# Performance work log

Measured on AMD Instinct MI355X. Metric: run time of the kernel, lower is better.

The kernel has to match this reference:

```python
import jax, jax.numpy as jnp
import numpy as np

ITEM_NUM = 100000
H = 128          # hidden_size
L_PROTO = 500    # number of prototypes
K = 4            # top-k prototypes
SEQ = 50         # max_seq_length
B = 1024
TAO = 0.1
LAMBDA = 0.1
EPS = 1e-5


def layer_norm(x, g, b):
    mu = jnp.mean(x, axis=-1, keepdims=True)
    var = jnp.mean((x - mu) ** 2, axis=-1, keepdims=True)
    return (x - mu) * jax.lax.rsqrt(var + EPS) * g + b


def setup_inputs() -> dict:
    key = jax.random.key(0)
    ks = jax.random.split(key, 12)
    std = 0.02
    item_emb = jax.random.normal(ks[0], (ITEM_NUM, H), jnp.float32) * std
    item_emb = item_emb.at[0].set(0.0)  # padding_idx=0
    pos_emb = jax.random.normal(ks[1], (SEQ + 1, H), jnp.float32) * std
    pos_emb = pos_emb.at[0].set(0.0)    # padding_idx=0 (never hit when len==SEQ)
    proto = jax.random.normal(ks[2], (L_PROTO, H), jnp.float32) * std
    w1 = jax.random.normal(ks[3], (H, H), jnp.float32) * std
    w2 = jax.random.normal(ks[4], (H, 1), jnp.float32) * std
    w3 = jax.random.normal(ks[5], (H, H), jnp.float32) * std
    w4 = jax.random.normal(ks[6], (H, H), jnp.float32) * std
    w5 = jax.random.normal(ks[7], (H, K), jnp.float32) * std
    w6 = jax.random.normal(ks[8], (H, H), jnp.float32) * std
    w7 = jax.random.normal(ks[9], (H, 1), jnp.float32) * std
    seq = jax.random.randint(ks[10], (B, SEQ), 0, ITEM_NUM, dtype=jnp.int64)
    g = jnp.ones((H,), jnp.float32)
    b = jnp.zeros((H,), jnp.float32)
    return {
        'item_emb': item_emb, 'pos_emb': pos_emb, 'proto': proto,
        'w1': w1, 'w2': w2, 'w3': w3, 'w4': w4, 'w5': w5, 'w6': w6, 'w7': w7,
        'ln1_g': g, 'ln1_b': b, 'ln2_g': g, 'ln2_b': b,
        'ln3_g': g, 'ln3_b': b, 'ln4_g': g, 'ln4_b': b,
        'seq': seq,
    }


def reference(item_emb, pos_emb, proto, w1, w2, w3, w4, w5, w6, w7,
              ln1_g, ln1_b, ln2_g, ln2_b, ln3_g, ln3_b, ln4_g, ln4_b, seq):
    mask = (seq != 0).astype(jnp.float32)            # [B,S]
    ie = item_emb[seq]                               # [B,S,H]

    # self-attentive virtual concept vector
    sa_score = jnp.squeeze(jnp.tanh(ie @ w1) @ w2, -1)   # [B,S]
    sa_score = sa_score - (1.0 - mask) * 10000.0
    alpha = jax.nn.softmax(sa_score, axis=-1)
    vcv = jnp.einsum('bs,bsh->bh', alpha, ie)            # [B,H]

    # prototype routing: top-k by score
    s = vcv @ proto.T                                    # [B,L]
    chosen_s, rank = jax.lax.top_k(s, K)                 # [B,K]
    chosen_proto = proto[rank]                           # [B,K,H]
    chosen_proto = jax.nn.sigmoid(chosen_s)[..., None] * chosen_proto

    # item->prototype assignment
    p_kt_score = jnp.einsum('bsh,bkh->bsk',
                            layer_norm(ie @ w3, ln1_g, ln1_b),
                            layer_norm(chosen_proto, ln2_g, ln2_b))
    p_kt = jax.nn.softmax(p_kt_score, axis=-1) * mask[:, :, None]  # [B,S,K]

    # positional embedding (positions SEQ..1)
    position = SEQ - jnp.arange(SEQ)                     # [S]
    emb = pos_emb[position][None, :, :] + ie             # [B,S,H]

    a_k_score = jnp.swapaxes(jnp.tanh(emb @ w4) @ w5, 1, 2)   # [B,K,S]
    a_k = jax.nn.softmax(a_k_score, axis=-1) * mask[:, None, :]
    a_k = jnp.swapaxes(a_k, 1, 2)                        # [B,S,K]

    p = p_kt * a_k
    interesting = layer_norm(jnp.einsum('bsk,bsh->bkh', p, emb), ln3_g, ln3_b)  # [B,K,H]

    xu = jnp.einsum('bsk,bkh->bsh', p_kt, chosen_proto)  # [B,S,H]
    c_score = jnp.squeeze(jnp.tanh(xu @ w6) @ w7, -1) - (1.0 - mask) * 10000.0
    c_w = jax.nn.softmax(c_score, axis=-1)               # [B,S]
    c_apt = layer_norm(jnp.einsum('bs,bsh->bh', c_w, xu), ln4_g, ln4_b)  # [B,H]

    e_score = jnp.einsum('bh,bkh->bk', c_apt, interesting)
    e = jax.nn.softmax(e_score / TAO, axis=-1)
    final = jnp.einsum('bk,bkh->bh', e, interesting)     # [B,H]
    scores = final @ item_emb.T                          # [B,ITEM_NUM]

    # prototype covariance regularizer
    centered = proto - jnp.mean(proto, axis=0, keepdims=True)
    M = (centered @ centered.T) / H
    Lc = (jnp.linalg.norm(M) - jnp.linalg.norm(jnp.diag(M))) * 0.5
    return scores, LAMBDA * Lc
```

## Files before the change

kernel.cpp:

```cpp
#include <hip/hip_runtime.h>
#include <hip/hip_bf16.h>

#define H 128
#define H2 132
#define SQL 50
#define LPROTO 500
#define KTOP 4
#define BQ 1024
#define ITEMS 100000

typedef __attribute__((ext_vector_type(8))) short bf16x8;
typedef __attribute__((ext_vector_type(4))) float f32x4;

__device__ __forceinline__ float wsum(float v){
#pragma unroll
  for (int o = 32; o; o >>= 1) v += __shfl_xor(v, o, 64);
  return v;
}
__device__ __forceinline__ float wmax(float v){
#pragma unroll
  for (int o = 32; o; o >>= 1) v = fmaxf(v, __shfl_xor(v, o, 64));
  return v;
}
__device__ __forceinline__ float gr16(float v){
  v += __shfl_xor(v, 1, 64);
  v += __shfl_xor(v, 2, 64);
  v += __shfl_xor(v, 4, 64);
  v += __shfl_xor(v, 8, 64);
  return v;
}
__device__ __forceinline__ unsigned short f2bf(float x){
  unsigned int u = __builtin_bit_cast(unsigned int, x);
  unsigned int r = u + 0x7fffu + ((u >> 16) & 1u);
  return (unsigned short)(r >> 16);
}
__device__ __forceinline__ float bf2f(unsigned short h){
  unsigned int u = ((unsigned int)h) << 16;
  return __builtin_bit_cast(float, u);
}
__device__ __forceinline__ float ftanh(float x){
  float e = __expf(-2.0f * fabsf(x));
  float t = (1.0f - e) / (1.0f + e);
  return copysignf(t, x);
}

__device__ __forceinline__ void mm_core(const float xs[4][8],
                                        const unsigned short* __restrict__ wt_hi,
                                        const unsigned short* __restrict__ wt_lo,
                                        int r15, int kof, f32x4* acc)
{
  bf16x8 ah[4], al[4];
#pragma unroll
  for (int ks = 0; ks < 4; ks++){
    bf16x8 h, l;
#pragma unroll
    for (int e = 0; e < 8; e++){
      unsigned short hb = f2bf(xs[ks][e]);
      float rem = xs[ks][e] - bf2f(hb);
      h[e] = (short)hb;
      l[e] = (short)f2bf(rem);
    }
    ah[ks] = h; al[ks] = l;
  }
#pragma unroll
  for (int j = 0; j < 8; j++){
    const unsigned short* bp = wt_hi + (j * 16 + r15) * H + kof;
    const unsigned short* lp = wt_lo + (j * 16 + r15) * H + kof;
    f32x4 a = (f32x4){0.f, 0.f, 0.f, 0.f};
#pragma unroll
    for (int ks = 0; ks < 4; ks++){
      bf16x8 bh = *reinterpret_cast<const bf16x8*>(bp + ks * 32);
      bf16x8 bl = *reinterpret_cast<const bf16x8*>(lp + ks * 32);
      a = __builtin_amdgcn_mfma_f32_16x16x32_bf16(ah[ks], bh, a, 0, 0, 0);
      a = __builtin_amdgcn_mfma_f32_16x16x32_bf16(al[ks], bh, a, 0, 0, 0);
      a = __builtin_amdgcn_mfma_f32_16x16x32_bf16(ah[ks], bl, a, 0, 0, 0);
    }
    acc[j] = a;
  }
}

__device__ __forceinline__ void mm_acc(const float (*src)[H2],
                                       const unsigned short* __restrict__ wt_hi,
                                       const unsigned short* __restrict__ wt_lo,
                                       int lane, int wave, f32x4* acc)
{
  const int r15 = lane & 15, g = lane >> 4, kof = g * 8;
  const int row = wave * 16 + r15;
  const int srw = (row < SQL) ? row : 0;
  float xs[4][8];
#pragma unroll
  for (int ks = 0; ks < 4; ks++){
    const float* p = &src[srw][ks * 32 + kof];
    float4 x0 = *reinterpret_cast<const float4*>(p);
    float4 x1 = *reinterpret_cast<const float4*>(p + 4);
    xs[ks][0]=x0.x; xs[ks][1]=x0.y; xs[ks][2]=x0.z; xs[ks][3]=x0.w;
    xs[ks][4]=x1.x; xs[ks][5]=x1.y; xs[ks][6]=x1.z; xs[ks][7]=x1.w;
  }
  mm_core(xs, wt_hi, wt_lo, r15, kof, acc);
}

__device__ __forceinline__ void mm_acc_pos(const float (*src)[H2],
                                           const float* __restrict__ pos_emb,
                                           const unsigned short* __restrict__ wt_hi,
                                           const unsigned short* __restrict__ wt_lo,
                                           int lane, int wave, f32x4* acc)
{
  const int r15 = lane & 15, g = lane >> 4, kof = g * 8;
  const int row = wave * 16 + r15;
  const int srw = (row < SQL) ? row : 0;
  const float* pp = pos_emb + (SQL - srw) * H;
  float xs[4][8];
#pragma unroll
  for (int ks = 0; ks < 4; ks++){
    const float* p = &src[srw][ks * 32 + kof];
    float4 x0 = *reinterpret_cast<const float4*>(p);
    float4 x1 = *reinterpret_cast<const float4*>(p + 4);
    float4 p0 = *reinterpret_cast<const float4*>(pp + ks * 32 + kof);
    float4 p1 = *reinterpret_cast<const float4*>(pp + ks * 32 + kof + 4);
    xs[ks][0]=x0.x+p0.x; xs[ks][1]=x0.y+p0.y; xs[ks][2]=x0.z+p0.z; xs[ks][3]=x0.w+p0.w;
    xs[ks][4]=x1.x+p1.x; xs[ks][5]=x1.y+p1.y; xs[ks][6]=x1.z+p1.z; xs[ks][7]=x1.w+p1.w;
  }
  mm_core(xs, wt_hi, wt_lo, r15, kof, acc);
}

extern "C" __global__ __launch_bounds__(256, 4)
void sine_row(const float* __restrict__ item_emb, const float* __restrict__ pos_emb,
              const float* __restrict__ proto,
              const float* __restrict__ w2, const float* __restrict__ w5,
              const float* __restrict__ w7,
              const unsigned short* __restrict__ wt,
              const float* __restrict__ ln1g, const float* __restrict__ ln1b,
              const float* __restrict__ ln2g, const float* __restrict__ ln2b,
              const float* __restrict__ ln3g, const float* __restrict__ ln3b,
              const float* __restrict__ ln4g, const float* __restrict__ ln4b,
              const int* __restrict__ seq,
              unsigned short* __restrict__ finalbf)
{
  __shared__ __align__(16) float sA[SQL][H2];
  __shared__ __align__(16) float scp[KTOP][H];
  __shared__ __align__(16) float slncp[KTOP][H];
  __shared__ __align__(16) float sintr[KTOP][H];
  __shared__ __align__(16) float svcv[H];
  __shared__ __align__(16) float scapt[H];
  __shared__ float srow[SQL];
  __shared__ float smask[SQL];
  __shared__ float spkt[SQL][KTOP];
  __shared__ float sak[SQL][KTOP];
  __shared__ float ssc[LPROTO];
  __shared__ float schs[KTOP];
  __shared__ int   srank[KTOP];
  __shared__ float sesc[KTOP];

  const int b = blockIdx.x;
  const int t = threadIdx.x;
  const int lane = t & 63;
  const int wave = t >> 6;
  const int r15 = lane & 15;
  const int g   = lane >> 4;
  const int* sq = seq + b * SQL;

  const unsigned short* w1t_hi = wt;
  const unsigned short* w1t_lo = wt + 16384;
  const unsigned short* w3t_hi = wt + 32768;
  const unsigned short* w3t_lo = wt + 49152;
  const unsigned short* w4t_hi = wt + 65536;
  const unsigned short* w4t_lo = wt + 81920;
  const unsigned short* w6t_hi = wt + 98304;
  const unsigned short* w6t_lo = wt + 114688;

  if (t < SQL) smask[t] = (sq[t] != 0) ? 1.0f : 0.0f;
  for (int c = t; c < SQL * (H / 4); c += 256){
    int s = c >> 5, q = c & 31;
    int idx = sq[s];
    float4 v = reinterpret_cast<const float4*>(item_emb)[idx * (H / 4) + q];
    reinterpret_cast<float4*>(&sA[s][0])[q] = v;
  }
  __syncthreads();

  {
    f32x4 acc[8];
    mm_acc(sA, w1t_hi, w1t_lo, lane, wave, acc);
    float p0 = 0.f, p1 = 0.f, p2 = 0.f, p3 = 0.f;
#pragma unroll
    for (int j = 0; j < 8; j++){
      float w2c = w2[j * 16 + r15];
      p0 = fmaf(ftanh(acc[j][0]), w2c, p0);
      p1 = fmaf(ftanh(acc[j][1]), w2c, p1);
      p2 = fmaf(ftanh(acc[j][2]), w2c, p2);
      p3 = fmaf(ftanh(acc[j][3]), w2c, p3);
    }
    p0 = gr16(p0); p1 = gr16(p1); p2 = gr16(p2); p3 = gr16(p3);
    if (r15 == 0){
      float pv[4] = {p0, p1, p2, p3};
#pragma unroll
      for (int r = 0; r < 4; r++){
        int orow = wave * 16 + g * 4 + r;
        if (orow < SQL) srow[orow] = pv[r] - (1.0f - smask[orow]) * 10000.0f;
      }
    }
  }
  __syncthreads();

  if (wave == 0){
    float v = (lane < SQL) ? srow[lane] : -1e30f;
    float m = wmax(v);
    float e = (lane < SQL) ? __expf(v - m) : 0.0f;
    float sum = wsum(e);
    if (lane < SQL) srow[lane] = e / sum;
  }
  __syncthreads();
  if (t < H){
    float acc = 0.f;
    for (int s = 0; s < SQL; s++) acc = fmaf(srow[s], sA[s][t], acc);
    svcv[t] = acc;
  }
  __syncthreads();

  for (int l = t; l < LPROTO; l += 256){
    const float4* pr = reinterpret_cast<const float4*>(proto + l * H);
    const float4* vc = reinterpret_cast<const float4*>(svcv);
    float acc = 0.f;
    for (int q = 0; q < H / 4; q++){
      float4 p = pr[q], v = vc[q];
      acc += p.x * v.x + p.y * v.y + p.z * v.z + p.w * v.w;
    }
    ssc[l] = acc;
  }
  __syncthreads();
  if (wave == 0){
    float cand[8];
#pragma unroll
    for (int i = 0; i < 8; i++){
      int l = lane + 64 * i;
      cand[i] = (l < LPROTO) ? ssc[l] : -1e30f;
    }
    for (int k = 0; k < KTOP; k++){
      float bv = -1e30f; int bi = 0x7fffffff;
#pragma unroll
      for (int i = 0; i < 8; i++){
        int l = lane + 64 * i;
        if (cand[i] > bv || (cand[i] == bv && l < bi)){ bv = cand[i]; bi = l; }
      }
#pragma unroll
      for (int o = 32; o; o >>= 1){
        float ov = __shfl_xor(bv, o, 64);
        int   oi = __shfl_xor(bi, o, 64);
        if (ov > bv || (ov == bv && oi < bi)){ bv = ov; bi = oi; }
      }
      if (lane == 0){ schs[k] = bv; srank[k] = bi; }
      int li = bi - lane;
#pragma unroll
      for (int i = 0; i < 8; i++) if (64 * i == li) cand[i] = -1e30f;
    }
  }
  __syncthreads();
  {
    int k = wave;
    int r = srank[k];
    float sg = 1.0f / (1.0f + __expf(-schs[k]));
    float v0 = sg * proto[r * H + lane];
    float v1 = sg * proto[r * H + 64 + lane];
    float mu = wsum(v0 + v1) * (1.0f / H);
    float d0 = v0 - mu, d1 = v1 - mu;
    float var = wsum(d0 * d0 + d1 * d1) * (1.0f / H);
    float rs = rsqrtf(var + 1e-5f);
    scp[k][lane] = v0; scp[k][64 + lane] = v1;
    slncp[k][lane]      = d0 * rs * ln2g[lane]      + ln2b[lane];
    slncp[k][64 + lane] = d1 * rs * ln2g[64 + lane] + ln2b[64 + lane];
  }
  __syncthreads();

  {
    f32x4 acc[8];
    mm_acc(sA, w3t_hi, w3t_lo, lane, wave, acc);
    float s0 = 0.f, s1 = 0.f, s2 = 0.f, s3 = 0.f;
#pragma unroll
    for (int j = 0; j < 8; j++){ s0 += acc[j][0]; s1 += acc[j][1]; s2 += acc[j][2]; s3 += acc[j][3]; }
    float mu0 = gr16(s0) * (1.0f / H), mu1 = gr16(s1) * (1.0f / H);
    float mu2 = gr16(s2) * (1.0f / H), mu3 = gr16(s3) * (1.0f / H);
    float q0 = 0.f, q1 = 0.f, q2 = 0.f, q3 = 0.f;
#pragma unroll
    for (int j = 0; j < 8; j++){
      float d0 = acc[j][0] - mu0, d1 = acc[j][1] - mu1;
      float d2 = acc[j][2] - mu2, d3 = acc[j][3] - mu3;
      q0 = fmaf(d0, d0, q0); q1 = fmaf(d1, d1, q1);
      q2 = fmaf(d2, d2, q2); q3 = fmaf(d3, d3, q3);
    }
    float rs0 = rsqrtf(gr16(q0) * (1.0f / H) + 1e-5f);
    float rs1 = rsqrtf(gr16(q1) * (1.0f / H) + 1e-5f);
    float rs2 = rsqrtf(gr16(q2) * (1.0f / H) + 1e-5f);
    float rs3 = rsqrtf(gr16(q3) * (1.0f / H) + 1e-5f);
    float pk[4][4];
#pragma unroll
    for (int k = 0; k < 4; k++)
#pragma unroll
      for (int r = 0; r < 4; r++) pk[k][r] = 0.f;
#pragma unroll
    for (int j = 0; j < 8; j++){
      int c = j * 16 + r15;
      float gg = ln1g[c], bb = ln1b[c];
      float l0 = fmaf((acc[j][0] - mu0) * rs0, gg, bb);
      float l1 = fmaf((acc[j][1] - mu1) * rs1, gg, bb);
      float l2 = fmaf((acc[j][2] - mu2) * rs2, gg, bb);
      float l3 = fmaf((acc[j][3] - mu3) * rs3, gg, bb);
#pragma unroll
      for (int k = 0; k < 4; k++){
        float w = slncp[k][c];
        pk[k][0] = fmaf(l0, w, pk[k][0]);
        pk[k][1] = fmaf(l1, w, pk[k][1]);
        pk[k][2] = fmaf(l2, w, pk[k][2]);
        pk[k][3] = fmaf(l3, w, pk[k][3]);
      }
    }
#pragma unroll
    for (int k = 0; k < 4; k++)
#pragma unroll
      for (int r = 0; r < 4; r++) pk[k][r] = gr16(pk[k][r]);
    if (r15 == 0){
#pragma unroll
      for (int r = 0; r < 4; r++){
        int orow = wave * 16 + g * 4 + r;
        if (orow < SQL){
          float m = fmaxf(fmaxf(pk[0][r], pk[1][r]), fmaxf(pk[2][r], pk[3][r]));
          float e0 = __expf(pk[0][r] - m), e1 = __expf(pk[1][r] - m);
          float e2 = __expf(pk[2][r] - m), e3 = __expf(pk[3][r] - m);
          float inv = 1.0f / (e0 + e1 + e2 + e3);
          float msk = smask[orow];
          spkt[orow][0] = e0 * inv * msk; spkt[orow][1] = e1 * inv * msk;
          spkt[orow][2] = e2 * inv * msk; spkt[orow][3] = e3 * inv * msk;
        }
      }
    }
  }
  __syncthreads();

  {
    f32x4 acc[8];
    mm_acc_pos(sA, pos_emb, w4t_hi, w4t_lo, lane, wave, acc);
    float pk[4][4];
#pragma unroll
    for (int k = 0; k < 4; k++)
#pragma unroll
      for (int r = 0; r < 4; r++) pk[k][r] = 0.f;
#pragma unroll
    for (int j = 0; j < 8; j++){
      int c = j * 16 + r15;
      float4 w5c = *reinterpret_cast<const float4*>(w5 + c * 4);
      float t0 = ftanh(acc[j][0]), t1 = ftanh(acc[j][1]);
      float t2 = ftanh(acc[j][2]), t3 = ftanh(acc[j][3]);
      pk[0][0] = fmaf(t0, w5c.x, pk[0][0]); pk[0][1] = fmaf(t1, w5c.x, pk[0][1]);
      pk[0][2] = fmaf(t2, w5c.x, pk[0][2]); pk[0][3] = fmaf(t3, w5c.x, pk[0][3]);
      pk[1][0] = fmaf(t0, w5c.y, pk[1][0]); pk[1][1] = fmaf(t1, w5c.y, pk[1][1]);
      pk[1][2] = fmaf(t2, w5c.y, pk[1][2]); pk[1][3] = fmaf(t3, w5c.y, pk[1][3]);
      pk[2][0] = fmaf(t0, w5c.z, pk[2][0]); pk[2][1] = fmaf(t1, w5c.z, pk[2][1]);
      pk[2][2] = fmaf(t2, w5c.z, pk[2][2]); pk[2][3] = fmaf(t3, w5c.z, pk[2][3]);
      pk[3][0] = fmaf(t0, w5c.w, pk[3][0]); pk[3][1] = fmaf(t1, w5c.w, pk[3][1]);
      pk[3][2] = fmaf(t2, w5c.w, pk[3][2]); pk[3][3] = fmaf(t3, w5c.w, pk[3][3]);
    }
#pragma unroll
    for (int k = 0; k < 4; k++)
#pragma unroll
      for (int r = 0; r < 4; r++) pk[k][r] = gr16(pk[k][r]);
    if (r15 == 0){
#pragma unroll
      for (int r = 0; r < 4; r++){
        int orow = wave * 16 + g * 4 + r;
        if (orow < SQL){
          sak[orow][0] = pk[0][r]; sak[orow][1] = pk[1][r];
          sak[orow][2] = pk[2][r]; sak[orow][3] = pk[3][r];
        }
      }
    }
  }
  __syncthreads();

  {
    int k = wave;
    float v = (lane < SQL) ? sak[lane][k] : -1e30f;
    float m = wmax(v);
    float e = (lane < SQL) ? __expf(v - m) : 0.0f;
    float sum = wsum(e);
    if (lane < SQL) sak[lane][k] = (e / sum) * smask[lane] * spkt[lane][k];
  }
  __syncthreads();

  for (int c = t; c < KTOP * H; c += 256){
    int k = c >> 7, h = c & 127;
    float acc = 0.f;
    for (int s = 0; s < SQL; s++)
      acc = fmaf(sak[s][k], sA[s][h] + pos_emb[(SQL - s) * H + h], acc);
    sintr[k][h] = acc;
  }
  __syncthreads();
  {
    int k = wave;
    float v0 = sintr[k][lane], v1 = sintr[k][64 + lane];
    float mu = wsum(v0 + v1) * (1.0f / H);
    float d0 = v0 - mu, d1 = v1 - mu;
    float var = wsum(d0 * d0 + d1 * d1) * (1.0f / H);
    float rs = rsqrtf(var + 1e-5f);
    sintr[k][lane]      = d0 * rs * ln3g[lane]      + ln3b[lane];
    sintr[k][64 + lane] = d1 * rs * ln3g[64 + lane] + ln3b[64 + lane];
  }
  __syncthreads();

  for (int c = t; c < SQL * H; c += 256){
    int s = c >> 7, h = c & 127;
    float acc = spkt[s][0] * scp[0][h] + spkt[s][1] * scp[1][h]
              + spkt[s][2] * scp[2][h] + spkt[s][3] * scp[3][h];
    sA[s][h] = acc;
  }
  __syncthreads();
  {
    f32x4 acc[8];
    mm_acc(sA, w6t_hi, w6t_lo, lane, wave, acc);
    float p0 = 0.f, p1 = 0.f, p2 = 0.f, p3 = 0.f;
#pragma unroll
    for (int j = 0; j < 8; j++){
      float w7c = w7[j * 16 + r15];
      p0 = fmaf(ftanh(acc[j][0]), w7c, p0);
      p1 = fmaf(ftanh(acc[j][1]), w7c, p1);
      p2 = fmaf(ftanh(acc[j][2]), w7c, p2);
      p3 = fmaf(ftanh(acc[j][3]), w7c, p3);
    }
    p0 = gr16(p0); p1 = gr16(p1); p2 = gr16(p2); p3 = gr16(p3);
    if (r15 == 0){
      float pv[4] = {p0, p1, p2, p3};
#pragma unroll
      for (int r = 0; r < 4; r++){
        int orow = wave * 16 + g * 4 + r;
        if (orow < SQL) srow[orow] = pv[r] - (1.0f - smask[orow]) * 10000.0f;
      }
    }
  }
  __syncthreads();

  if (wave == 0){
    float v = (lane < SQL) ? srow[lane] : -1e30f;
    float m = wmax(v);
    float e = (lane < SQL) ? __expf(v - m) : 0.0f;
    float sum = wsum(e);
    if (lane < SQL) srow[lane] = e / sum;
  }
  __syncthreads();
  if (t < H){
    float acc = 0.f;
    for (int s = 0; s < SQL; s++) acc = fmaf(srow[s], sA[s][t], acc);
    scapt[t] = acc;
  }
  __syncthreads();
  if (wave == 0){
    float v0 = scapt[lane], v1 = scapt[64 + lane];
    float mu = wsum(v0 + v1) * (1.0f / H);
    float d0 = v0 - mu, d1 = v1 - mu;
    float var = wsum(d0 * d0 + d1 * d1) * (1.0f / H);
    float rs = rsqrtf(var + 1e-5f);
    scapt[lane]      = d0 * rs * ln4g[lane]      + ln4b[lane];
    scapt[64 + lane] = d1 * rs * ln4g[64 + lane] + ln4b[64 + lane];
  }
  __syncthreads();

  {
    int k = wave;
    float part = scapt[lane] * sintr[k][lane] + scapt[64 + lane] * sintr[k][64 + lane];
    float sc = wsum(part);
    if (lane == 0) sesc[k] = sc;
  }
  __syncthreads();
  if (t < H){
    float e0 = sesc[0] * 10.0f, e1 = sesc[1] * 10.0f, e2 = sesc[2] * 10.0f, e3 = sesc[3] * 10.0f;
    float m = fmaxf(fmaxf(e0, e1), fmaxf(e2, e3));
    float x0 = __expf(e0 - m), x1 = __expf(e1 - m), x2 = __expf(e2 - m), x3 = __expf(e3 - m);
    float inv = 1.0f / (x0 + x1 + x2 + x3);
    float f = (x0 * sintr[0][t] + x1 * sintr[1][t] + x2 * sintr[2][t] + x3 * sintr[3][t]) * inv;
    finalbf[b * H + t] = f2bf(f);
  }
}

extern "C" __global__ void wprep(const float* __restrict__ w1, const float* __restrict__ w3,
                                 const float* __restrict__ w4, const float* __restrict__ w6,
                                 unsigned short* __restrict__ out){
  const float* srcs[4] = {w1, w3, w4, w6};
  const float* src = srcs[blockIdx.x];
  unsigned short* hi = out + blockIdx.x * 32768;
  unsigned short* lo = hi + 16384;
  for (int i = threadIdx.x; i < 16384; i += 256){
    int c = i >> 7, k = i & 127;
    float f = src[k * H + c];
    unsigned short h = f2bf(f);
    hi[i] = h;
    lo[i] = f2bf(f - bf2f(h));
  }
}

extern "C" __global__ void conv_bf16(const float* __restrict__ in,
                                     unsigned short* __restrict__ out, int n4){
  int i = blockIdx.x * blockDim.x + threadIdx.x;
  int stride = gridDim.x * blockDim.x;
  for (; i < n4; i += stride){
    float4 v = reinterpret_cast<const float4*>(in)[i];
    union { unsigned short u[4]; uint2 v2; } o;
    o.u[0] = f2bf(v.x); o.u[1] = f2bf(v.y); o.u[2] = f2bf(v.z); o.u[3] = f2bf(v.w);
    reinterpret_cast<uint2*>(out)[i] = o.v2;
  }
}

#define GBN 128
#define LDT 136

extern "C" __global__ __launch_bounds__(256)
void gemm_scores(const unsigned short* __restrict__ A,
                 const unsigned short* __restrict__ Bm,
                 float* __restrict__ C)
{
  __shared__ __align__(16) unsigned short sB[GBN][LDT];
  const int t = threadIdx.x, lane = t & 63, wave = t >> 6;
  const int r15 = lane & 15, g = lane >> 4;
  const int n0 = blockIdx.x * GBN;

  for (int c = t; c < GBN * 16; c += 256){
    int r = c >> 4, q = c & 15;
    int n = n0 + r;
    uint4 v = make_uint4(0u, 0u, 0u, 0u);
    if (n < ITEMS) v = reinterpret_cast<const uint4*>(Bm + (size_t)n * H)[q];
    *reinterpret_cast<uint4*>(&sB[r][q * 8]) = v;
  }
  __syncthreads();

  for (int mt = 0; mt < BQ / 128; mt++){
    const int m0 = mt * 128 + wave * 32;
    f32x4 acc[2][8];
#pragma unroll
    for (int i = 0; i < 2; i++)
#pragma unroll
      for (int j = 0; j < 8; j++) acc[i][j] = (f32x4){0.f, 0.f, 0.f, 0.f};

#pragma unroll
    for (int ks = 0; ks < 4; ks++){
      bf16x8 af[2];
#pragma unroll
      for (int i = 0; i < 2; i++)
        af[i] = *reinterpret_cast<const bf16x8*>(A + (m0 + i * 16 + r15) * H + ks * 32 + g * 8);
#pragma unroll
      for (int j = 0; j < 8; j++){
        bf16x8 bfr = *reinterpret_cast<const bf16x8*>(&sB[j * 16 + r15][ks * 32 + g * 8]);
        acc[0][j] = __builtin_amdgcn_mfma_f32_16x16x32_bf16(af[0], bfr, acc[0][j], 0, 0, 0);
        acc[1][j] = __builtin_amdgcn_mfma_f32_16x16x32_bf16(af[1], bfr, acc[1][j], 0, 0, 0);
      }
    }

#pragma unroll
    for (int i = 0; i < 2; i++){
      int mrow = m0 + i * 16 + g * 4;
#pragma unroll
      for (int j = 0; j < 8; j++){
        int nc = n0 + j * 16 + r15;
        if (nc < ITEMS){
#pragma unroll
          for (int r = 0; r < 4; r++)
            C[(size_t)(mrow + r) * ITEMS + nc] = acc[i][j][r];
        }
      }
    }
  }
}

extern "C" __global__ void proto_mean(const float* __restrict__ proto,
                                      float* __restrict__ mean, float* __restrict__ accum){
  __shared__ float part[4][H];
  int t = threadIdx.x;
  int h = t & 127, p = t >> 7;
  if (t < 2) accum[t] = 0.0f;
  float acc = 0.f;
  for (int l = p; l < LPROTO; l += 4) acc += proto[l * H + h];
  part[p][h] = acc;
  __syncthreads();
  if (t < H) mean[t] = (part[0][t] + part[1][t] + part[2][t] + part[3][t]) * (1.0f / LPROTO);
}

extern "C" __global__ __launch_bounds__(256)
void proto_cov(const float* __restrict__ proto, const float* __restrict__ mean,
               float* __restrict__ accum){
  __shared__ float ci[H];
  __shared__ float cm[H];
  __shared__ float red[256];
  int i = blockIdx.x, t = threadIdx.x;
  if (t < H){ cm[t] = mean[t]; ci[t] = proto[i * H + t] - mean[t]; }
  __syncthreads();
  float total = 0.f;
  for (int j = t; j < LPROTO; j += 256){
    float acc = 0.f;
    for (int h = 0; h < H; h++) acc = fmaf(ci[h], proto[j * H + h] - cm[h], acc);
    float m = acc * (1.0f / H);
    total += m * m;
    if (j == i) atomicAdd(&accum[1], m * m);
  }
  red[t] = total; __syncthreads();
  for (int o = 128; o; o >>= 1){ if (t < o) red[t] += red[t + o]; __syncthreads(); }
  if (t == 0) atomicAdd(&accum[0], red[0]);
}

extern "C" __global__ void lc_final(const float* __restrict__ accum, float* __restrict__ out){
  out[(size_t)BQ * ITEMS] = 0.1f * 0.5f * (sqrtf(accum[0]) - sqrtf(accum[1]));
}

extern "C" void kernel_launch(void* const* d_in, const int* in_sizes, int n_in,
                              void* d_out, int out_size, void* d_ws, size_t ws_size,
                              hipStream_t stream){
  const float* item  = (const float*)d_in[0];
  const float* pos   = (const float*)d_in[1];
  const float* proto = (const float*)d_in[2];
  const float* w1 = (const float*)d_in[3];
  const float* w2 = (const float*)d_in[4];
  const float* w3 = (const float*)d_in[5];
  const float* w4 = (const float*)d_in[6];
  const float* w5 = (const float*)d_in[7];
  const float* w6 = (const float*)d_in[8];
  const float* w7 = (const float*)d_in[9];
  const float* ln1g = (const float*)d_in[10];
  const float* ln1b = (const float*)d_in[11];
  const float* ln2g = (const float*)d_in[12];
  const float* ln2b = (const float*)d_in[13];
  const float* ln3g = (const float*)d_in[14];
  const float* ln3b = (const float*)d_in[15];
  const float* ln4g = (const float*)d_in[16];
  const float* ln4b = (const float*)d_in[17];
  const int* seq = (const int*)d_in[18];
  float* out = (float*)d_out;

  char* ws = (char*)d_ws;
  float* accum = (float*)ws;
  float* mean  = (float*)(ws + 256);
  unsigned short* finalbf = (unsigned short*)(ws + 1024);
  unsigned short* itembf  = (unsigned short*)(ws + 263168);
  unsigned short* wtbuf   = (unsigned short*)(ws + 25863168);

  wprep<<<4, 256, 0, stream>>>(w1, w3, w4, w6, wtbuf);
  conv_bf16<<<2048, 256, 0, stream>>>(item, itembf, ITEMS * H / 4);

  sine_row<<<BQ, 256, 0, stream>>>(item, pos, proto, w2, w5, w7, wtbuf,
                                   ln1g, ln1b, ln2g, ln2b, ln3g, ln3b, ln4g, ln4b,
                                   seq, finalbf);

  gemm_scores<<<dim3((ITEMS + GBN - 1) / GBN), 256, 0, stream>>>(finalbf, itembf, out);

  proto_mean<<<1, 512, 0, stream>>>(proto, mean, accum);
  proto_cov<<<LPROTO, 256, 0, stream>>>(proto, mean, accum);
  lc_final<<<1, 1, 0, stream>>>(accum, out);
}
```

Baseline: 390.4 us.

## Tile score GEMM in 2D with shared-memory A tile and 64x64 wave tiles

The score GEMM previously launched one block per 128-item column strip and looped over all 1024 query rows, reading A fragments directly from global memory. It now launches a 2D grid of 128x128 output tiles, stages both A and B tiles in shared memory, and gives each wave a 64x64 sub-tile with a 4x4 MFMA accumulator block. This raises parallelism (about 8x more blocks) and register-level operand reuse. The cost is that each item-embedding tile is now loaded once per M-tile, eight times in total, and the kernel uses more LDS per block.

```diff
diff --git a/kernel.cpp b/kernel.cpp
--- a/kernel.cpp
+++ b/kernel.cpp
@@ -505,6 +505,7 @@
   }
 }
 
+#define GBM 128
 #define GBN 128
 #define LDT 136
 
@@ -513,11 +514,18 @@
                  const unsigned short* __restrict__ Bm,
                  float* __restrict__ C)
 {
+  __shared__ __align__(16) unsigned short sA[GBM][LDT];
   __shared__ __align__(16) unsigned short sB[GBN][LDT];
   const int t = threadIdx.x, lane = t & 63, wave = t >> 6;
   const int r15 = lane & 15, g = lane >> 4;
   const int n0 = blockIdx.x * GBN;
-
+  const int m0 = blockIdx.y * GBM;
+
+  for (int c = t; c < GBM * 16; c += 256){
+    int r = c >> 4, q = c & 15;
+    uint4 v = reinterpret_cast<const uint4*>(A + (m0 + r) * H)[q];
+    *reinterpret_cast<uint4*>(&sA[r][q * 8]) = v;
+  }
   for (int c = t; c < GBN * 16; c += 256){
     int r = c >> 4, q = c & 15;
     int n = n0 + r;
@@ -527,39 +535,39 @@
   }
   __syncthreads();
 
-  for (int mt = 0; mt < BQ / 128; mt++){
-    const int m0 = mt * 128 + wave * 32;
-    f32x4 acc[2][8];
-#pragma unroll
-    for (int i = 0; i < 2; i++)
-#pragma unroll
-      for (int j = 0; j < 8; j++) acc[i][j] = (f32x4){0.f, 0.f, 0.f, 0.f};
-
-#pragma unroll
-    for (int ks = 0; ks < 4; ks++){
-      bf16x8 af[2];
-#pragma unroll
-      for (int i = 0; i < 2; i++)
-        af[i] = *reinterpret_cast<const bf16x8*>(A + (m0 + i * 16 + r15) * H + ks * 32 + g * 8);
-#pragma unroll
-      for (int j = 0; j < 8; j++){
-        bf16x8 bfr = *reinterpret_cast<const bf16x8*>(&sB[j * 16 + r15][ks * 32 + g * 8]);
-        acc[0][j] = __builtin_amdgcn_mfma_f32_16x16x32_bf16(af[0], bfr, acc[0][j], 0, 0, 0);
-        acc[1][j] = __builtin_amdgcn_mfma_f32_16x16x32_bf16(af[1], bfr, acc[1][j], 0, 0, 0);
-      }
-    }
-
-#pragma unroll
-    for (int i = 0; i < 2; i++){
-      int mrow = m0 + i * 16 + g * 4;
-#pragma unroll
-      for (int j = 0; j < 8; j++){
-        int nc = n0 + j * 16 + r15;
-        if (nc < ITEMS){
-#pragma unroll
-          for (int r = 0; r < 4; r++)
-            C[(size_t)(mrow + r) * ITEMS + nc] = acc[i][j][r];
-        }
+  const int wm = wave >> 1, wn = wave & 1;
+  f32x4 acc[4][4];
+#pragma unroll
+  for (int i = 0; i < 4; i++)
+#pragma unroll
+    for (int j = 0; j < 4; j++) acc[i][j] = (f32x4){0.f, 0.f, 0.f, 0.f};
+
+#pragma unroll
+  for (int ks = 0; ks < 4; ks++){
+    bf16x8 af[4], bfr[4];
+#pragma unroll
+    for (int i = 0; i < 4; i++)
+      af[i] = *reinterpret_cast<const bf16x8*>(&sA[wm * 64 + i * 16 + r15][ks * 32 + g * 8]);
+#pragma unroll
+    for (int j = 0; j < 4; j++)
+      bfr[j] = *reinterpret_cast<const bf16x8*>(&sB[wn * 64 + j * 16 + r15][ks * 32 + g * 8]);
+#pragma unroll
+    for (int i = 0; i < 4; i++)
+#pragma unroll
+      for (int j = 0; j < 4; j++)
+        acc[i][j] = __builtin_amdgcn_mfma_f32_16x16x32_bf16(af[i], bfr[j], acc[i][j], 0, 0, 0);
+  }
+
+#pragma unroll
+  for (int i = 0; i < 4; i++){
+    int mrow = m0 + wm * 64 + i * 16 + g * 4;
+#pragma unroll
+    for (int j = 0; j < 4; j++){
+      int ncol = n0 + wn * 64 + j * 16 + r15;
+      if (ncol < ITEMS){
+#pragma unroll
+        for (int r = 0; r < 4; r++)
+          C[(size_t)(mrow + r) * ITEMS + ncol] = acc[i][j][r];
       }
     }
   }
@@ -642,7 +650,7 @@
                                    ln1g, ln1b, ln2g, ln2b, ln3g, ln3b, ln4g, ln4b,
                                    seq, finalbf);
 
-  gemm_scores<<<dim3((ITEMS + GBN - 1) / GBN), 256, 0, stream>>>(finalbf, itembf, out);
+  gemm_scores<<<dim3((ITEMS + GBN - 1) / GBN, BQ / GBM), 256, 0, stream>>>(finalbf, itembf, out);
 
   proto_mean<<<1, 512, 0, stream>>>(proto, mean, accum);
   proto_cov<<<LPROTO, 256, 0, stream>>>(proto, mean, accum);
```

Result: slower. 400.8 us (+2.7%).
